# Performance work log

Hardware: AMD Instinct MI355X
Metric: run time of the kernel (lower is better)

The kernel has to match this reference:

```python
import jax, jax.numpy as jnp
import numpy as np
from jax.scipy.special import logsumexp

N, T, C, H, V = 8, 512, 1024, 256, 32000


def _res_layer(x, W1, b1, W2, b2):
    # hmm-lm ResLayer: x + ReLU(Linear(ReLU(Linear(x))))
    return x + jax.nn.relu(jax.nn.relu(x @ W1.T + b1) @ W2.T + b2)


def setup_inputs() -> dict:
    key = jax.random.key(0)
    ks = jax.random.split(key, 12)
    g = lambda k, shape: jax.random.normal(k, shape, jnp.float32) * (1.0 / np.sqrt(shape[-1]))
    return {
        "text": jax.random.randint(ks[0], (N, T), 0, V),
        "start_emb": jax.random.normal(ks[1], (H,), jnp.float32),
        "start_lin_W": g(ks[2], (H, H)),
        "start_lin_b": jnp.zeros((H,), jnp.float32),
        "start_res_W1": g(ks[3], (2, H, H)),
        "start_res_b1": jnp.zeros((2, H), jnp.float32),
        "start_res_W2": g(ks[4], (2, H, H)),
        "start_res_b2": jnp.zeros((2, H), jnp.float32),
        "state_emb": g(ks[5], (C, H)),
        "next_state_emb": g(ks[6], (C, H)),
        "preterminal_emb": g(ks[7], (C, H)),
        "term_res_W1": g(ks[8], (2, H, H)),
        "term_res_b1": jnp.zeros((2, H), jnp.float32),
        "term_res_W2": g(ks[9], (2, H, H)),
        "term_res_b2": jnp.zeros((2, H), jnp.float32),
        "terminal_emb": g(ks[10], (V, H)),
    }


def reference(text, start_emb, start_lin_W, start_lin_b,
              start_res_W1, start_res_b1, start_res_W2, start_res_b2,
              state_emb, next_state_emb, preterminal_emb,
              term_res_W1, term_res_b1, term_res_W2, term_res_b2,
              terminal_emb):
    # --- start distribution: start_mlp(start_emb) @ next_state_emb.T (tie_start) ---
    fx = start_emb @ start_lin_W.T + start_lin_b
    for i in range(2):
        fx = _res_layer(fx, start_res_W1[i], start_res_b1[i], start_res_W2[i], start_res_b2[i])
    start = jax.nn.log_softmax(fx @ next_state_emb.T)            # [C]

    # --- transition: log_softmax(state_emb @ next_state_emb.T) ---
    transition = jax.nn.log_softmax(state_emb @ next_state_emb.T, axis=-1)  # [C, C]

    # --- emission: log_softmax(terminal_mlp(preterminal_emb) @ terminal_emb.T) ---
    ft = preterminal_emb
    for i in range(2):
        ft = _res_layer(ft, term_res_W1[i], term_res_b1[i], term_res_W2[i], term_res_b2[i])
    emission = jax.nn.log_softmax(ft @ terminal_emb.T, axis=-1)  # [C, V]
    emis_t = emission.T                                          # [V, C]

    # --- HMM forward (log-space) scan; evidence = logsumexp(alpha_T) summed over batch ---
    alpha0 = start[None, :] + emis_t[text[:, 0]]                 # [N, C]

    def step(alpha, x_t):
        # alpha: [N, C]; x_t: [N]
        a = logsumexp(alpha[:, :, None] + transition[None], axis=1) + emis_t[x_t]
        return a, None

    alpha_T, _ = jax.lax.scan(step, alpha0, text[:, 1:].T)       # time-major [T-1, N]
    evidence = logsumexp(alpha_T, axis=-1).sum()
    return evidence
```

## Files before the change

kernel.cpp:

```cpp
#include <hip/hip_runtime.h>
#include <stdint.h>
#include <stddef.h>

#define N_ 8
#define T_ 512
#define C_ 1024
#define H_ 256
#define V_ 32000

#define OFF_START   0u
#define OFF_LSE     4096u
#define OFF_EVP     8192u
#define OFF_FT      81920u
#define OFF_P       1130496u
#define OFF_PART    5324800u
#define OFF_EEXP    5849088u
#define OFF_BUF     22626304u
#define OFF_FLAGS   22724608u

typedef __attribute__((ext_vector_type(8))) short short8;
typedef __attribute__((ext_vector_type(4))) float floatx4;

__device__ __forceinline__ float dot4(float4 a, float4 b) {
  return a.x*b.x + a.y*b.y + a.z*b.z + a.w*b.w;
}

__device__ __forceinline__ unsigned short f2bf(float f) {
  unsigned u = __float_as_uint(f);
  unsigned r = u + 0x7fffu + ((u >> 16) & 1u);
  return (unsigned short)(r >> 16);
}

__device__ __forceinline__ unsigned pk_bf2(float x, float y) {
  return ((unsigned)f2bf(y) << 16) | (unsigned)f2bf(x);
}

__device__ __forceinline__ short8 pack8(float4 a, float4 b) {
  union { short8 s; unsigned u[4]; } r;
  r.u[0] = pk_bf2(a.x, a.y);
  r.u[1] = pk_bf2(a.z, a.w);
  r.u[2] = pk_bf2(b.x, b.y);
  r.u[3] = pk_bf2(b.z, b.w);
  return r.s;
}

__global__ __launch_bounds__(256) void k_start(
    const float* __restrict__ se, const float* __restrict__ lw, const float* __restrict__ lb,
    const float* __restrict__ W1, const float* __restrict__ b1,
    const float* __restrict__ W2, const float* __restrict__ b2,
    const float* __restrict__ nse, float* __restrict__ out_start)
{
  __shared__ float xs[H_], fx[H_], h1[H_];
  __shared__ float lg[C_];
  __shared__ float redk[4];
  int tid = threadIdx.x;
  xs[tid] = se[tid];
  __syncthreads();
  {
    float acc = lb[tid];
    const float4* wr = (const float4*)(lw + (size_t)tid*H_);
    for (int k = 0; k < H_/4; ++k) acc += dot4(wr[k], *(const float4*)&xs[k*4]);
    fx[tid] = acc;
  }
  __syncthreads();
  for (int L = 0; L < 2; ++L) {
    {
      float acc = b1[L*H_ + tid];
      const float4* wr = (const float4*)(W1 + (size_t)(L*H_ + tid)*H_);
      for (int k = 0; k < H_/4; ++k) acc += dot4(wr[k], *(const float4*)&fx[k*4]);
      h1[tid] = fmaxf(acc, 0.f);
    }
    __syncthreads();
    {
      float acc = b2[L*H_ + tid];
      const float4* wr = (const float4*)(W2 + (size_t)(L*H_ + tid)*H_);
      for (int k = 0; k < H_/4; ++k) acc += dot4(wr[k], *(const float4*)&h1[k*4]);
      fx[tid] += fmaxf(acc, 0.f);
    }
    __syncthreads();
  }
  float lmax = -1e30f;
  for (int r = 0; r < 4; ++r) {
    int cc = tid + r*256;
    float acc = 0.f;
    const float4* er = (const float4*)(nse + (size_t)cc*H_);
    for (int k = 0; k < H_/4; ++k) acc += dot4(er[k], *(const float4*)&fx[k*4]);
    lg[cc] = acc;
    lmax = fmaxf(lmax, acc);
  }
  for (int m = 32; m; m >>= 1) lmax = fmaxf(lmax, __shfl_xor(lmax, m, 64));
  if ((tid & 63) == 0) redk[tid >> 6] = lmax;
  __syncthreads();
  float M = fmaxf(fmaxf(redk[0], redk[1]), fmaxf(redk[2], redk[3]));
  __syncthreads();
  float ssum = 0.f;
  for (int r = 0; r < 4; ++r) ssum += __expf(lg[tid + r*256] - M);
  for (int m = 32; m; m >>= 1) ssum += __shfl_xor(ssum, m, 64);
  if ((tid & 63) == 0) redk[tid >> 6] = ssum;
  __syncthreads();
  float S = redk[0] + redk[1] + redk[2] + redk[3];
  float lse = M + __logf(S);
  for (int r = 0; r < 4; ++r) {
    int cc = tid + r*256;
    out_start[cc] = lg[cc] - lse;
  }
}

__global__ __launch_bounds__(256) void k_gemm_cc(
    const float* __restrict__ A, const float* __restrict__ B, float* __restrict__ Cout)
{
  __shared__ float As[64][69];
  __shared__ float Bs[64][69];
  int tid = threadIdx.x;
  int bi = blockIdx.y, bj = blockIdx.x;
  int sr = tid >> 2, sq = tid & 3;
  int tx = tid & 15, ty = tid >> 4;
  float acc[4][4] = {};
  for (int kb = 0; kb < H_; kb += 64) {
    __syncthreads();
    {
      const float* ar = A + (size_t)(bi*64 + sr)*H_ + kb + sq*16;
      const float* br = B + (size_t)(bj*64 + sr)*H_ + kb + sq*16;
#pragma unroll
      for (int qq = 0; qq < 4; ++qq) {
        float4 av = *(const float4*)(ar + qq*4);
        float4 bv = *(const float4*)(br + qq*4);
        int kk = sq*16 + qq*4;
        As[sr][kk+0]=av.x; As[sr][kk+1]=av.y; As[sr][kk+2]=av.z; As[sr][kk+3]=av.w;
        Bs[sr][kk+0]=bv.x; Bs[sr][kk+1]=bv.y; Bs[sr][kk+2]=bv.z; Bs[sr][kk+3]=bv.w;
      }
    }
    __syncthreads();
#pragma unroll 4
    for (int k = 0; k < 64; ++k) {
      float a0 = As[ty*4+0][k], a1 = As[ty*4+1][k], a2 = As[ty*4+2][k], a3 = As[ty*4+3][k];
      float b0 = Bs[tx*4+0][k], b1 = Bs[tx*4+1][k], b2 = Bs[tx*4+2][k], b3 = Bs[tx*4+3][k];
      acc[0][0]+=a0*b0; acc[0][1]+=a0*b1; acc[0][2]+=a0*b2; acc[0][3]+=a0*b3;
      acc[1][0]+=a1*b0; acc[1][1]+=a1*b1; acc[1][2]+=a1*b2; acc[1][3]+=a1*b3;
      acc[2][0]+=a2*b0; acc[2][1]+=a2*b1; acc[2][2]+=a2*b2; acc[2][3]+=a2*b3;
      acc[3][0]+=a3*b0; acc[3][1]+=a3*b1; acc[3][2]+=a3*b2; acc[3][3]+=a3*b3;
    }
  }
#pragma unroll
  for (int ii = 0; ii < 4; ++ii)
#pragma unroll
    for (int jj = 0; jj < 4; ++jj)
      Cout[(size_t)(bi*64 + ty*4 + ii)*C_ + bj*64 + tx*4 + jj] = acc[ii][jj];
}

__global__ __launch_bounds__(256) void k_softmax_rows(float* __restrict__ P)
{
  __shared__ float redk[4];
  int row = blockIdx.x, tid = threadIdx.x;
  float4* pr = (float4*)(P + (size_t)row*C_);
  float4 v = pr[tid];
  float m = fmaxf(fmaxf(v.x, v.y), fmaxf(v.z, v.w));
  for (int mm = 32; mm; mm >>= 1) m = fmaxf(m, __shfl_xor(m, mm, 64));
  if ((tid & 63) == 0) redk[tid >> 6] = m;
  __syncthreads();
  float M = fmaxf(fmaxf(redk[0], redk[1]), fmaxf(redk[2], redk[3]));
  __syncthreads();
  float4 e;
  e.x = __expf(v.x - M); e.y = __expf(v.y - M); e.z = __expf(v.z - M); e.w = __expf(v.w - M);
  float s = e.x + e.y + e.z + e.w;
  for (int mm = 32; mm; mm >>= 1) s += __shfl_xor(s, mm, 64);
  if ((tid & 63) == 0) redk[tid >> 6] = s;
  __syncthreads();
  float S = redk[0] + redk[1] + redk[2] + redk[3];
  float inv = 1.0f / S;
  e.x *= inv; e.y *= inv; e.z *= inv; e.w *= inv;
  pr[tid] = e;
}

__global__ __launch_bounds__(256) void k_mlp(
    const float* __restrict__ inp, const float* __restrict__ W1, const float* __restrict__ b1,
    const float* __restrict__ W2, const float* __restrict__ b2, float* __restrict__ ft)
{
  __shared__ float xs[4][H_];
  __shared__ float hs[4][H_];
  int tid = threadIdx.x;
  int r0 = blockIdx.x * 4;
  int lr = tid >> 6, lc = (tid & 63) * 4;
  *(float4*)&xs[lr][lc] = *(const float4*)(inp + (size_t)(r0+lr)*H_ + lc);
  __syncthreads();
  for (int L = 0; L < 2; ++L) {
    {
      const float4* wr = (const float4*)(W1 + (size_t)(L*H_ + tid)*H_);
      float bb = b1[L*H_ + tid];
      float a0=bb, a1=bb, a2=bb, a3=bb;
      for (int k = 0; k < H_/4; ++k) {
        float4 w = wr[k];
        a0 += dot4(w, *(const float4*)&xs[0][k*4]);
        a1 += dot4(w, *(const float4*)&xs[1][k*4]);
        a2 += dot4(w, *(const float4*)&xs[2][k*4]);
        a3 += dot4(w, *(const float4*)&xs[3][k*4]);
      }
      hs[0][tid]=fmaxf(a0,0.f); hs[1][tid]=fmaxf(a1,0.f);
      hs[2][tid]=fmaxf(a2,0.f); hs[3][tid]=fmaxf(a3,0.f);
    }
    __syncthreads();
    {
      const float4* wr = (const float4*)(W2 + (size_t)(L*H_ + tid)*H_);
      float bb = b2[L*H_ + tid];
      float a0=bb, a1=bb, a2=bb, a3=bb;
      for (int k = 0; k < H_/4; ++k) {
        float4 w = wr[k];
        a0 += dot4(w, *(const float4*)&hs[0][k*4]);
        a1 += dot4(w, *(const float4*)&hs[1][k*4]);
        a2 += dot4(w, *(const float4*)&hs[2][k*4]);
        a3 += dot4(w, *(const float4*)&hs[3][k*4]);
      }
      xs[0][tid] += fmaxf(a0,0.f); xs[1][tid] += fmaxf(a1,0.f);
      xs[2][tid] += fmaxf(a2,0.f); xs[3][tid] += fmaxf(a3,0.f);
    }
    __syncthreads();
  }
  *(float4*)(ft + (size_t)(r0+lr)*H_ + lc) = *(float4*)&xs[lr][lc];
}

#define LSE_VSPLIT 16
#define LSE_VPB    2000
#define LSE_CHUNKS 125

__global__ __launch_bounds__(256) void k_lse_mfma(
    const float* __restrict__ ft, const float* __restrict__ emb, float* __restrict__ part)
{
  int tid = threadIdx.x;
  int lane = tid & 63;
  int w = tid >> 6;
  int q = blockIdx.x;
  int jb = blockIdx.y * 64 + w * 16;
  int r16 = lane & 15, kb = lane >> 4;

  short8 A[8];
  {
    const float* arow = ft + (size_t)(jb + r16) * H_ + kb * 8;
#pragma unroll
    for (int ks = 0; ks < 8; ++ks) {
      float4 a = *(const float4*)(arow + ks * 32);
      float4 b = *(const float4*)(arow + ks * 32 + 4);
      A[ks] = pack8(a, b);
    }
  }
  float s0 = 0.f, s1 = 0.f, s2 = 0.f, s3 = 0.f;
  const float* embq = emb + (size_t)q * LSE_VPB * H_;
#pragma unroll 1
  for (int ch = 0; ch < LSE_CHUNKS; ++ch) {
    const float* brow = embq + (size_t)(ch * 16 + r16) * H_ + kb * 8;
    floatx4 acca = {0,0,0,0}, accb = {0,0,0,0};
#pragma unroll
    for (int ks = 0; ks < 8; ks += 2) {
      float4 x0 = *(const float4*)(brow + ks * 32);
      float4 y0 = *(const float4*)(brow + ks * 32 + 4);
      float4 x1 = *(const float4*)(brow + ks * 32 + 32);
      float4 y1 = *(const float4*)(brow + ks * 32 + 36);
      acca = __builtin_amdgcn_mfma_f32_16x16x32_bf16(A[ks],   pack8(x0, y0), acca, 0, 0, 0);
      accb = __builtin_amdgcn_mfma_f32_16x16x32_bf16(A[ks+1], pack8(x1, y1), accb, 0, 0, 0);
    }
    s0 += __expf(acca[0] + accb[0]);
    s1 += __expf(acca[1] + accb[1]);
    s2 += __expf(acca[2] + accb[2]);
    s3 += __expf(acca[3] + accb[3]);
  }
#pragma unroll
  for (int mm = 1; mm <= 8; mm <<= 1) {
    s0 += __shfl_xor(s0, mm, 64);
    s1 += __shfl_xor(s1, mm, 64);
    s2 += __shfl_xor(s2, mm, 64);
    s3 += __shfl_xor(s3, mm, 64);
  }
  if (r16 == 0) {
    int jrow = jb + kb * 4;
    part[(size_t)(jrow + 0) * LSE_VSPLIT + q] = s0;
    part[(size_t)(jrow + 1) * LSE_VSPLIT + q] = s1;
    part[(size_t)(jrow + 2) * LSE_VSPLIT + q] = s2;
    part[(size_t)(jrow + 3) * LSE_VSPLIT + q] = s3;
  }
}

__global__ __launch_bounds__(256) void k_lse_reduce(
    const float* __restrict__ part, float* __restrict__ lse_row)
{
  int row = blockIdx.x * 256 + threadIdx.x;
  const float4* p = (const float4*)(part + (size_t)row * LSE_VSPLIT);
  float4 a = p[0], b = p[1], c = p[2], d = p[3];
  float s = a.x+a.y+a.z+a.w + b.x+b.y+b.z+b.w + c.x+c.y+c.z+c.w + d.x+d.y+d.z+d.w;
  lse_row[row] = __logf(s);
}

__global__ __launch_bounds__(256) void k_eexp_mfma(
    const float* __restrict__ ft, const float* __restrict__ emb, const int* __restrict__ text,
    const float* __restrict__ lse_row, float* __restrict__ EEXP)
{
  int tid = threadIdx.x;
  int lane = tid & 63;
  int w = tid >> 6;
  int jb = blockIdx.y * 64 + w * 16;
  int tb = blockIdx.x * 64;
  int r16 = lane & 15, kb = lane >> 4;

  short8 A[8];
  {
    const float* arow = ft + (size_t)(jb + r16) * H_ + kb * 8;
#pragma unroll
    for (int ks = 0; ks < 8; ++ks) {
      float4 a = *(const float4*)(arow + ks * 32);
      float4 b = *(const float4*)(arow + ks * 32 + 4);
      A[ks] = pack8(a, b);
    }
  }
  float4 lsej = *(const float4*)(lse_row + jb + kb * 4);

#pragma unroll 1
  for (int tc = 0; tc < 4; ++tc) {
    int idx = tb + tc * 16 + r16;
    int tok = text[idx];
    const float* brow = emb + (size_t)tok * H_ + kb * 8;
    floatx4 acca = {0,0,0,0}, accb = {0,0,0,0};
#pragma unroll
    for (int ks = 0; ks < 8; ks += 2) {
      float4 x0 = *(const float4*)(brow + ks * 32);
      float4 y0 = *(const float4*)(brow + ks * 32 + 4);
      float4 x1 = *(const float4*)(brow + ks * 32 + 32);
      float4 y1 = *(const float4*)(brow + ks * 32 + 36);
      acca = __builtin_amdgcn_mfma_f32_16x16x32_bf16(A[ks],   pack8(x0, y0), acca, 0, 0, 0);
      accb = __builtin_amdgcn_mfma_f32_16x16x32_bf16(A[ks+1], pack8(x1, y1), accb, 0, 0, 0);
    }
    float4 o;
    o.x = __expf(acca[0] + accb[0] - lsej.x);
    o.y = __expf(acca[1] + accb[1] - lsej.y);
    o.z = __expf(acca[2] + accb[2] - lsej.z);
    o.w = __expf(acca[3] + accb[3] - lsej.w);
    *(float4*)(EEXP + (size_t)idx * C_ + jb + kb * 4) = o;
  }
}

#define SCAN_LDS 136352

__global__ __launch_bounds__(256) void k_scan(
    const float* __restrict__ P, const float* __restrict__ EEXP, const float* __restrict__ startv,
    float* __restrict__ bufG, unsigned* __restrict__ flagsG, float* __restrict__ evp)
{
  extern __shared__ char smem[];
  char*  Pl   = smem;
  char*  Pr   = smem + 65536;
  char*  Al   = smem + 131072;
  float* red  = (float*)(smem + 135168);
  char*  Ub   = smem + 136192;
  float* redm = (float*)(smem + 136320);

  int tid  = threadIdx.x;
  int bid  = blockIdx.x;
  int c    = bid >> 2;
  int ng   = bid & 3;
  int n0   = ng * 2;
  int lane = tid & 63;
  int w    = tid >> 6;
  int s    = tid >> 7;
  int k0   = (tid & 127) * 8;
  int r16  = lane & 15, kb = lane >> 4;
  int j0   = r16;
  int jswz = j0 << 4;

  unsigned* myflags = flagsG + ng*32;
  float* bufq[3];
  bufq[0] = bufG + (size_t)(0*4 + ng)*2048;
  bufq[1] = bufG + (size_t)(1*4 + ng)*2048;
  bufq[2] = bufG + (size_t)(2*4 + ng)*2048;

  {
    int j4 = (tid & 7) * 4;
    int irow = tid >> 3;
    for (int rep = 0; rep < 32; ++rep) {
      int i = rep*32 + irow;
      float4 v = *(const float4*)(P + (size_t)i*C_ + c*32 + j4);
      int ib = 2*i;
      *(unsigned short*)(Pl + (size_t)(j4+0)*2048 + (ib ^ (((j4+0)&15)<<4))) = f2bf(v.x);
      *(unsigned short*)(Pl + (size_t)(j4+1)*2048 + (ib ^ (((j4+1)&15)<<4))) = f2bf(v.y);
      *(unsigned short*)(Pl + (size_t)(j4+2)*2048 + (ib ^ (((j4+2)&15)<<4))) = f2bf(v.z);
      *(unsigned short*)(Pl + (size_t)(j4+3)*2048 + (ib ^ (((j4+3)&15)<<4))) = f2bf(v.w);
    }
  }
  {
    int jb4 = (tid & 255) * 4;
    for (int m = 0; m < 32; ++m) {
      float4 v = *(const float4*)(P + (size_t)(c*32 + m)*C_ + jb4);
#pragma unroll
      for (int dj = 0; dj < 4; ++dj) {
        int j = jb4 + dj;
        float vv = (dj==0)?v.x:(dj==1)?v.y:(dj==2)?v.z:v.w;
        *(unsigned short*)(Pr + (size_t)(j>>4)*1024 + (j&15)*64 + m*2) = f2bf(vv);
      }
    }
  }

  float ls = 0.f;

#pragma unroll 1
  for (int r = 0; r < 256; ++r) {
    float ue = 0.f;
    if (tid < 64) {
      int ss = tid >> 5, col = tid & 31;
      ue = EEXP[((size_t)(n0+ss)*T_ + (2*r+1))*C_ + c*32 + col];
    }

    float av[8];
    if (r == 0) {
#pragma unroll
      for (int j = 0; j < 8; ++j)
        av[j] = __expf(startv[k0+j]) * EEXP[((size_t)(n0+s)*T_ + 0)*C_ + k0+j];
    } else {
      int guard = 0;
      for (;;) {
        unsigned f = (lane < 32)
          ? __hip_atomic_load(myflags + lane, __ATOMIC_RELAXED, __HIP_MEMORY_SCOPE_AGENT)
          : (unsigned)r;
        if (__ballot(f == (unsigned)r) == ~0ull) break;
        __builtin_amdgcn_s_sleep(1);
        if (++guard > 2000000) break;
      }
      float* srcb = bufq[(r-1)%3] + s*1024 + k0;
      float sv[8];
#pragma unroll
      for (int j = 0; j < 8; ++j)
        sv[j] = __hip_atomic_load(srcb + j, __ATOMIC_RELAXED, __HIP_MEMORY_SCOPE_AGENT);
      float4 e0 = *(const float4*)(EEXP + ((size_t)(n0+s)*T_ + 2*r)*C_ + k0);
      float4 e1 = *(const float4*)(EEXP + ((size_t)(n0+s)*T_ + 2*r)*C_ + k0 + 4);
      av[0]=sv[0]*e0.x; av[1]=sv[1]*e0.y; av[2]=sv[2]*e0.z; av[3]=sv[3]*e0.w;
      av[4]=sv[4]*e1.x; av[5]=sv[5]*e1.y; av[6]=sv[6]*e1.z; av[7]=sv[7]*e1.w;
      if (tid < 64) {
        int ss = tid >> 5, col = tid & 31;
        __hip_atomic_store(bufq[(r+1)%3] + ss*1024 + c*32 + col, 0.0f,
                           __ATOMIC_RELAXED, __HIP_MEMORY_SCOPE_AGENT);
      }
    }

    float m = fmaxf(fmaxf(fmaxf(av[0],av[1]),fmaxf(av[2],av[3])),
                    fmaxf(fmaxf(av[4],av[5]),fmaxf(av[6],av[7])));
#pragma unroll
    for (int mm = 1; mm <= 32; mm <<= 1) m = fmaxf(m, __shfl_xor(m, mm, 64));
    if (lane == 0) redm[w] = m;
    __syncthreads();
    float M = fmaxf(redm[s*2], redm[s*2+1]);
    ls += __logf(M);
    float rinv = 1.0f / M;
    {
      unsigned pk[4];
      pk[0] = pk_bf2(av[0]*rinv, av[1]*rinv);
      pk[1] = pk_bf2(av[2]*rinv, av[3]*rinv);
      pk[2] = pk_bf2(av[4]*rinv, av[5]*rinv);
      pk[3] = pk_bf2(av[6]*rinv, av[7]*rinv);
      int blk = k0 >> 5;
      *(uint4*)(Al + blk*128 + s*64 + (((k0&31)*2) ^ ((blk&3)<<4))) = *(const uint4*)pk;
    }
    __syncthreads();

    floatx4 acc0 = {0,0,0,0}, acc1 = {0,0,0,0};
#pragma unroll
    for (int b = 0; b < 8; ++b) {
      int blk = w*8 + b;
      short8 af = *(const short8*)(Al + blk*128 + (r16&1)*64 + ((kb*16) ^ ((blk&3)<<4)));
      int kby = 2*(blk*32 + kb*8);
      short8 f0 = *(const short8*)(Pl + (size_t)j0*2048 + (kby ^ jswz));
      short8 f1 = *(const short8*)(Pl + (size_t)(16+j0)*2048 + (kby ^ jswz));
      acc0 = __builtin_amdgcn_mfma_f32_16x16x32_bf16(af, f0, acc0, 0, 0, 0);
      acc1 = __builtin_amdgcn_mfma_f32_16x16x32_bf16(af, f1, acc1, 0, 0, 0);
    }
    if (lane < 16) {
      red[((w*2+0)*2+0)*16 + j0] = acc0[0];
      red[((w*2+0)*2+1)*16 + j0] = acc0[1];
      red[((w*2+1)*2+0)*16 + j0] = acc1[0];
      red[((w*2+1)*2+1)*16 + j0] = acc1[1];
    }
    __syncthreads();

    if (r == 255) {
      if (tid < 64) {
        int ss = tid >> 5, col = tid & 31;
        int tl = col >> 4, c16 = col & 15;
        float usum = red[((0*2+tl)*2+ss)*16 + c16] + red[((1*2+tl)*2+ss)*16 + c16]
                   + red[((2*2+tl)*2+ss)*16 + c16] + red[((3*2+tl)*2+ss)*16 + c16];
        (void)__hip_atomic_fetch_add(bufq[255%3] + ss*1024 + c*32 + col, usum * ue,
                                     __ATOMIC_RELAXED, __HIP_MEMORY_SCOPE_AGENT);
      }
      __syncthreads();
      if (tid == 0)
        __hip_atomic_store(myflags + c, 256u, __ATOMIC_RELAXED, __HIP_MEMORY_SCOPE_AGENT);
    } else {
      if (tid < 64) {
        int ss = tid >> 5, col = tid & 31;
        int tl = col >> 4, c16 = col & 15;
        float usum = red[((0*2+tl)*2+ss)*16 + c16] + red[((1*2+tl)*2+ss)*16 + c16]
                   + red[((2*2+tl)*2+ss)*16 + c16] + red[((3*2+tl)*2+ss)*16 + c16];
        *(unsigned short*)(Ub + ss*64 + col*2) = f2bf(usum * ue);
      }
      __syncthreads();
      short8 au = *(const short8*)(Ub + (r16&1)*64 + kb*16);
      float* bufp = bufq[r%3];
#pragma unroll 4
      for (int i = 0; i < 16; ++i) {
        int jt = w*16 + i;
        short8 bf = *(const short8*)(Pr + (size_t)jt*1024 + j0*64 + kb*16);
        floatx4 a = {0,0,0,0};
        a = __builtin_amdgcn_mfma_f32_16x16x32_bf16(au, bf, a, 0, 0, 0);
        if (lane < 16) {
          (void)__hip_atomic_fetch_add(bufp + 0*1024 + jt*16 + j0, a[0],
                                       __ATOMIC_RELAXED, __HIP_MEMORY_SCOPE_AGENT);
          (void)__hip_atomic_fetch_add(bufp + 1*1024 + jt*16 + j0, a[1],
                                       __ATOMIC_RELAXED, __HIP_MEMORY_SCOPE_AGENT);
        }
      }
      __syncthreads();
      if (tid == 0)
        __hip_atomic_store(myflags + c, (unsigned)(r+1), __ATOMIC_RELAXED, __HIP_MEMORY_SCOPE_AGENT);
    }
  }

  if (c == 0) {
    int guard = 0;
    for (;;) {
      unsigned f = (lane < 32)
        ? __hip_atomic_load(myflags + lane, __ATOMIC_RELAXED, __HIP_MEMORY_SCOPE_AGENT)
        : 256u;
      if (__ballot(f == 256u) == ~0ull) break;
      __builtin_amdgcn_s_sleep(1);
      if (++guard > 2000000) break;
    }
    float* srcb = bufq[255%3] + s*1024 + k0;
    float ssum = 0.f;
#pragma unroll
    for (int j = 0; j < 8; ++j)
      ssum += __hip_atomic_load(srcb + j, __ATOMIC_RELAXED, __HIP_MEMORY_SCOPE_AGENT);
#pragma unroll
    for (int mm = 1; mm <= 32; mm <<= 1) ssum += __shfl_xor(ssum, mm, 64);
    if (lane == 0) redm[w] = ssum;
    __syncthreads();
    if (tid == 0)   evp[n0]     = ls + __logf(redm[0] + redm[1]);
    if (tid == 128) evp[n0 + 1] = ls + __logf(redm[2] + redm[3]);
  }
}

__global__ void k_final(const float* __restrict__ evp, float* __restrict__ out)
{
  if (threadIdx.x == 0) {
    float s = 0.f;
#pragma unroll
    for (int i = 0; i < N_; ++i) s += evp[i];
    out[0] = s;
  }
}

extern "C" void kernel_launch(void* const* d_in, const int* in_sizes, int n_in,
                              void* d_out, int out_size, void* d_ws, size_t ws_size,
                              hipStream_t stream)
{
  const int*   text      = (const int*)  d_in[0];
  const float* start_emb = (const float*)d_in[1];
  const float* slw       = (const float*)d_in[2];
  const float* slb       = (const float*)d_in[3];
  const float* sW1       = (const float*)d_in[4];
  const float* sb1       = (const float*)d_in[5];
  const float* sW2       = (const float*)d_in[6];
  const float* sb2       = (const float*)d_in[7];
  const float* state_emb = (const float*)d_in[8];
  const float* nse       = (const float*)d_in[9];
  const float* pre_emb   = (const float*)d_in[10];
  const float* tW1       = (const float*)d_in[11];
  const float* tb1       = (const float*)d_in[12];
  const float* tW2       = (const float*)d_in[13];
  const float* tb2       = (const float*)d_in[14];
  const float* term_emb  = (const float*)d_in[15];

  char* ws = (char*)d_ws;
  float*    w_start = (float*)   (ws + OFF_START);
  float*    w_lse   = (float*)   (ws + OFF_LSE);
  float*    w_evp   = (float*)   (ws + OFF_EVP);
  float*    w_ft    = (float*)   (ws + OFF_FT);
  float*    w_P     = (float*)   (ws + OFF_P);
  float*    w_part  = (float*)   (ws + OFF_PART);
  float*    w_eexp  = (float*)   (ws + OFF_EEXP);
  float*    w_buf   = (float*)   (ws + OFF_BUF);
  unsigned* w_flags = (unsigned*)(ws + OFF_FLAGS);

  (void)hipMemsetAsync(ws + OFF_BUF, 0, 98304 + 512, stream);

  k_start<<<1, 256, 0, stream>>>(start_emb, slw, slb, sW1, sb1, sW2, sb2, nse, w_start);
  k_gemm_cc<<<dim3(16,16), 256, 0, stream>>>(state_emb, nse, w_P);
  k_softmax_rows<<<C_, 256, 0, stream>>>(w_P);
  k_mlp<<<C_/4, 256, 0, stream>>>(pre_emb, tW1, tb1, tW2, tb2, w_ft);
  k_lse_mfma<<<dim3(LSE_VSPLIT, 16), 256, 0, stream>>>(w_ft, term_emb, w_part);
  k_lse_reduce<<<4, 256, 0, stream>>>(w_part, w_lse);
  k_eexp_mfma<<<dim3(64, 16), 256, 0, stream>>>(w_ft, term_emb, text, w_lse, w_eexp);

  (void)hipFuncSetAttribute((const void*)k_scan, hipFuncAttributeMaxDynamicSharedMemorySize, SCAN_LDS);
  k_scan<<<128, 256, SCAN_LDS, stream>>>(w_P, w_eexp, w_start, w_buf, w_flags, w_evp);
  k_final<<<1, 64, 0, stream>>>(w_evp, (float*)d_out);
}
```

Before: 1.654 ms.

## Halve scan blocks, pre-pack transposed bf16 transition, use counter barrier and deferred max

Adds a kernel that writes the softmaxed transition matrix as a transposed bf16 copy. The scan now runs on 64 blocks of 64 columns each instead of 128 blocks of 32, and loads its slices straight from that copy. The right-hand operand is held in registers rather than LDS. The per-block flag array becomes a single atomic counter per batch group, and normalisation uses the previous step's max so one block-wide sync leaves the critical path. Fewer blocks cut the cross-block synchronisation cost per step, but each block does twice the work, and register pressure goes up from the 32 short8 register fragments.

```diff
diff --git a/kernel.cpp b/kernel.cpp
--- a/kernel.cpp
+++ b/kernel.cpp
@@ -16,7 +16,8 @@
 #define OFF_PART    5324800u
 #define OFF_EEXP    5849088u
 #define OFF_BUF     22626304u
-#define OFF_FLAGS   22724608u
+#define OFF_CNT     22724608u
+#define OFF_PT      22725120u
 
 typedef __attribute__((ext_vector_type(8))) short short8;
 typedef __attribute__((ext_vector_type(4))) float floatx4;
@@ -170,6 +171,32 @@
   float inv = 1.0f / S;
   e.x *= inv; e.y *= inv; e.z *= inv; e.w *= inv;
   pr[tid] = e;
+}
+
+__global__ __launch_bounds__(256) void k_packT(
+    const float* __restrict__ P, unsigned short* __restrict__ PT)
+{
+  __shared__ float ts[64][68];
+  int tid = threadIdx.x;
+  int bi = blockIdx.y, bj = blockIdx.x;
+  int rl = tid >> 4;
+  int cl4 = (tid & 15) * 4;
+#pragma unroll
+  for (int rr = 0; rr < 4; ++rr) {
+    int row = rr*16 + rl;
+    float4 v = *(const float4*)(P + (size_t)(bi*64 + row)*C_ + bj*64 + cl4);
+    ts[row][cl4+0]=v.x; ts[row][cl4+1]=v.y; ts[row][cl4+2]=v.z; ts[row][cl4+3]=v.w;
+  }
+  __syncthreads();
+  int jl = tid >> 2;
+  int m0 = (tid & 3) * 16;
+  unsigned pk[8];
+#pragma unroll
+  for (int u = 0; u < 8; ++u)
+    pk[u] = pk_bf2(ts[m0 + u*2][jl], ts[m0 + u*2 + 1][jl]);
+  char* dst = (char*)(PT + (size_t)(bj*64 + jl)*1024 + bi*64 + m0);
+  *(uint4*)(dst +  0) = *(const uint4*)&pk[0];
+  *(uint4*)(dst + 16) = *(const uint4*)&pk[4];
 }
 
 __global__ __launch_bounds__(256) void k_mlp(
@@ -335,19 +362,18 @@
   }
 }
 
-#define SCAN_LDS 136352
+#define SCAN_LDS (131072 + 4096 + 256 + 32)
 
 __global__ __launch_bounds__(256) void k_scan(
-    const float* __restrict__ P, const float* __restrict__ EEXP, const float* __restrict__ startv,
-    float* __restrict__ bufG, unsigned* __restrict__ flagsG, float* __restrict__ evp)
+    const unsigned short* __restrict__ PT, const float* __restrict__ EEXP,
+    const float* __restrict__ startv,
+    float* __restrict__ bufG, unsigned* __restrict__ cntG, float* __restrict__ evp)
 {
   extern __shared__ char smem[];
   char*  Pl   = smem;
-  char*  Pr   = smem + 65536;
   char*  Al   = smem + 131072;
-  float* red  = (float*)(smem + 135168);
-  char*  Ub   = smem + 136192;
-  float* redm = (float*)(smem + 136320);
+  char*  Ub   = smem + 135168;
+  float* redm = (float*)(smem + 135424);
 
   int tid  = threadIdx.x;
   int bid  = blockIdx.x;
@@ -358,92 +384,90 @@
   int w    = tid >> 6;
   int s    = tid >> 7;
   int k0   = (tid & 127) * 8;
-  int r16  = lane & 15, kb = lane >> 4;
-  int j0   = r16;
-  int jswz = j0 << 4;
-
-  unsigned* myflags = flagsG + ng*32;
+  int r16  = lane & 15;
+  int kb4  = lane >> 4;
+
+  unsigned* cnt = cntG + ng * 16;
   float* bufq[3];
   bufq[0] = bufG + (size_t)(0*4 + ng)*2048;
   bufq[1] = bufG + (size_t)(1*4 + ng)*2048;
   bufq[2] = bufG + (size_t)(2*4 + ng)*2048;
 
   {
-    int j4 = (tid & 7) * 4;
-    int irow = tid >> 3;
-    for (int rep = 0; rep < 32; ++rep) {
-      int i = rep*32 + irow;
-      float4 v = *(const float4*)(P + (size_t)i*C_ + c*32 + j4);
-      int ib = 2*i;
-      *(unsigned short*)(Pl + (size_t)(j4+0)*2048 + (ib ^ (((j4+0)&15)<<4))) = f2bf(v.x);
-      *(unsigned short*)(Pl + (size_t)(j4+1)*2048 + (ib ^ (((j4+1)&15)<<4))) = f2bf(v.y);
-      *(unsigned short*)(Pl + (size_t)(j4+2)*2048 + (ib ^ (((j4+2)&15)<<4))) = f2bf(v.z);
-      *(unsigned short*)(Pl + (size_t)(j4+3)*2048 + (ib ^ (((j4+3)&15)<<4))) = f2bf(v.w);
-    }
-  }
-  {
-    int jb4 = (tid & 255) * 4;
-    for (int m = 0; m < 32; ++m) {
-      float4 v = *(const float4*)(P + (size_t)(c*32 + m)*C_ + jb4);
-#pragma unroll
-      for (int dj = 0; dj < 4; ++dj) {
-        int j = jb4 + dj;
-        float vv = (dj==0)?v.x:(dj==1)?v.y:(dj==2)?v.z:v.w;
-        *(unsigned short*)(Pr + (size_t)(j>>4)*1024 + (j&15)*64 + m*2) = f2bf(vv);
-      }
-    }
-  }
-
-  float ls = 0.f;
+    int col = tid & 63, q = tid >> 6;
+    const char* src = (const char*)(PT + (size_t)(c*64 + col)*1024) + q*512;
+    char* dstb = Pl + (size_t)col*2048;
+    int swz = (col & 15) << 4;
+#pragma unroll
+    for (int u = 0; u < 32; ++u)
+      *(uint4*)(dstb + ((q*512 + u*16) ^ swz)) = *(const uint4*)(src + u*16);
+  }
+
+  short8 vb[16][2];
+#pragma unroll
+  for (int i = 0; i < 16; ++i)
+#pragma unroll
+    for (int q = 0; q < 2; ++q)
+      vb[i][q] = *(const short8*)((const char*)PT +
+          ((size_t)((w*16 + i)*16 + r16)*1024 + c*64 + q*32 + kb4*8)*2);
+
+  __syncthreads();
+
+  float ls   = 0.f;
+  float Muse = 1.f;
+  int s2   = r16 & 1;
+  int ucol = c*64 + w*16 + r16;
 
 #pragma unroll 1
   for (int r = 0; r < 256; ++r) {
-    float ue = 0.f;
-    if (tid < 64) {
-      int ss = tid >> 5, col = tid & 31;
-      ue = EEXP[((size_t)(n0+ss)*T_ + (2*r+1))*C_ + c*32 + col];
-    }
+    float ue0 = 0.f, ue1 = 0.f;
+    if (lane < 16) {
+      ue0 = EEXP[((size_t)(n0+0)*T_ + (2*r+1))*C_ + ucol];
+      ue1 = EEXP[((size_t)(n0+1)*T_ + (2*r+1))*C_ + ucol];
+    }
+    float4 e0 = *(const float4*)(EEXP + ((size_t)(n0+s)*T_ + 2*r)*C_ + k0);
+    float4 e1 = *(const float4*)(EEXP + ((size_t)(n0+s)*T_ + 2*r)*C_ + k0 + 4);
 
     float av[8];
     if (r == 0) {
-#pragma unroll
-      for (int j = 0; j < 8; ++j)
-        av[j] = __expf(startv[k0+j]) * EEXP[((size_t)(n0+s)*T_ + 0)*C_ + k0+j];
+      av[0] = __expf(startv[k0+0]) * e0.x;
+      av[1] = __expf(startv[k0+1]) * e0.y;
+      av[2] = __expf(startv[k0+2]) * e0.z;
+      av[3] = __expf(startv[k0+3]) * e0.w;
+      av[4] = __expf(startv[k0+4]) * e1.x;
+      av[5] = __expf(startv[k0+5]) * e1.y;
+      av[6] = __expf(startv[k0+6]) * e1.z;
+      av[7] = __expf(startv[k0+7]) * e1.w;
     } else {
+      unsigned tgt = 16u * (unsigned)r;
       int guard = 0;
       for (;;) {
-        unsigned f = (lane < 32)
-          ? __hip_atomic_load(myflags + lane, __ATOMIC_RELAXED, __HIP_MEMORY_SCOPE_AGENT)
-          : (unsigned)r;
-        if (__ballot(f == (unsigned)r) == ~0ull) break;
+        unsigned f = __hip_atomic_load(cnt, __ATOMIC_RELAXED, __HIP_MEMORY_SCOPE_AGENT);
+        if (f >= tgt) break;
         __builtin_amdgcn_s_sleep(1);
-        if (++guard > 2000000) break;
+        if (++guard > 4000000) break;
       }
       float* srcb = bufq[(r-1)%3] + s*1024 + k0;
       float sv[8];
 #pragma unroll
       for (int j = 0; j < 8; ++j)
         sv[j] = __hip_atomic_load(srcb + j, __ATOMIC_RELAXED, __HIP_MEMORY_SCOPE_AGENT);
-      float4 e0 = *(const float4*)(EEXP + ((size_t)(n0+s)*T_ + 2*r)*C_ + k0);
-      float4 e1 = *(const float4*)(EEXP + ((size_t)(n0+s)*T_ + 2*r)*C_ + k0 + 4);
       av[0]=sv[0]*e0.x; av[1]=sv[1]*e0.y; av[2]=sv[2]*e0.z; av[3]=sv[3]*e0.w;
       av[4]=sv[4]*e1.x; av[5]=sv[5]*e1.y; av[6]=sv[6]*e1.z; av[7]=sv[7]*e1.w;
-      if (tid < 64) {
-        int ss = tid >> 5, col = tid & 31;
-        __hip_atomic_store(bufq[(r+1)%3] + ss*1024 + c*32 + col, 0.0f,
+      if (tid < 128) {
+        int ss = tid >> 6, col = c*64 + (tid & 63);
+        __hip_atomic_store(bufq[(r+1)%3] + ss*1024 + col, 0.0f,
                            __ATOMIC_RELAXED, __HIP_MEMORY_SCOPE_AGENT);
       }
     }
 
-    float m = fmaxf(fmaxf(fmaxf(av[0],av[1]),fmaxf(av[2],av[3])),
-                    fmaxf(fmaxf(av[4],av[5]),fmaxf(av[6],av[7])));
-#pragma unroll
-    for (int mm = 1; mm <= 32; mm <<= 1) m = fmaxf(m, __shfl_xor(m, mm, 64));
-    if (lane == 0) redm[w] = m;
-    __syncthreads();
-    float M = fmaxf(redm[s*2], redm[s*2+1]);
-    ls += __logf(M);
-    float rinv = 1.0f / M;
+    ls += __logf(Muse);
+    float rinv = 1.0f / Muse;
+    float m8 = fmaxf(fmaxf(fmaxf(av[0],av[1]),fmaxf(av[2],av[3])),
+                     fmaxf(fmaxf(av[4],av[5]),fmaxf(av[6],av[7])));
+#pragma unroll
+    for (int mm = 1; mm <= 32; mm <<= 1) m8 = fmaxf(m8, __shfl_xor(m8, mm, 64));
+    if (lane == 0) redm[w] = m8;
     {
       unsigned pk[4];
       pk[0] = pk_bf2(av[0]*rinv, av[1]*rinv);
@@ -454,79 +478,73 @@
       *(uint4*)(Al + blk*128 + s*64 + (((k0&31)*2) ^ ((blk&3)<<4))) = *(const uint4*)pk;
     }
     __syncthreads();
-
-    floatx4 acc0 = {0,0,0,0}, acc1 = {0,0,0,0};
-#pragma unroll
-    for (int b = 0; b < 8; ++b) {
-      int blk = w*8 + b;
-      short8 af = *(const short8*)(Al + blk*128 + (r16&1)*64 + ((kb*16) ^ ((blk&3)<<4)));
-      int kby = 2*(blk*32 + kb*8);
-      short8 f0 = *(const short8*)(Pl + (size_t)j0*2048 + (kby ^ jswz));
-      short8 f1 = *(const short8*)(Pl + (size_t)(16+j0)*2048 + (kby ^ jswz));
-      acc0 = __builtin_amdgcn_mfma_f32_16x16x32_bf16(af, f0, acc0, 0, 0, 0);
-      acc1 = __builtin_amdgcn_mfma_f32_16x16x32_bf16(af, f1, acc1, 0, 0, 0);
-    }
-    if (lane < 16) {
-      red[((w*2+0)*2+0)*16 + j0] = acc0[0];
-      red[((w*2+0)*2+1)*16 + j0] = acc0[1];
-      red[((w*2+1)*2+0)*16 + j0] = acc1[0];
-      red[((w*2+1)*2+1)*16 + j0] = acc1[1];
-    }
-    __syncthreads();
+    Muse = fmaxf(fmaxf(redm[0], redm[1]), fmaxf(redm[2], redm[3])) * rinv;
+
+    floatx4 acc[4] = {{0,0,0,0},{0,0,0,0},{0,0,0,0},{0,0,0,0}};
+    {
+      const char* bcol = Pl + (size_t)(w*16 + r16)*2048;
+      int swzc = r16 << 4;
+#pragma unroll
+      for (int ch = 0; ch < 4; ++ch)
+#pragma unroll
+        for (int b8 = 0; b8 < 8; ++b8) {
+          int blk = b8*4 + ch;
+          short8 af = *(const short8*)(Al + blk*128 + s2*64 + ((kb4*16) ^ ((blk&3)<<4)));
+          short8 bf = *(const short8*)(bcol + ((blk*64 + kb4*16) ^ swzc));
+          acc[ch] = __builtin_amdgcn_mfma_f32_16x16x32_bf16(af, bf, acc[ch], 0, 0, 0);
+        }
+    }
+    floatx4 us;
+    us[0] = (acc[0][0]+acc[1][0]) + (acc[2][0]+acc[3][0]);
+    us[1] = (acc[0][1]+acc[1][1]) + (acc[2][1]+acc[3][1]);
 
     if (r == 255) {
-      if (tid < 64) {
-        int ss = tid >> 5, col = tid & 31;
-        int tl = col >> 4, c16 = col & 15;
-        float usum = red[((0*2+tl)*2+ss)*16 + c16] + red[((1*2+tl)*2+ss)*16 + c16]
-                   + red[((2*2+tl)*2+ss)*16 + c16] + red[((3*2+tl)*2+ss)*16 + c16];
-        (void)__hip_atomic_fetch_add(bufq[255%3] + ss*1024 + c*32 + col, usum * ue,
+      if (lane < 16) {
+        (void)__hip_atomic_fetch_add(bufq[0] + 0*1024 + ucol, us[0]*ue0,
+                                     __ATOMIC_RELAXED, __HIP_MEMORY_SCOPE_AGENT);
+        (void)__hip_atomic_fetch_add(bufq[0] + 1*1024 + ucol, us[1]*ue1,
                                      __ATOMIC_RELAXED, __HIP_MEMORY_SCOPE_AGENT);
       }
       __syncthreads();
       if (tid == 0)
-        __hip_atomic_store(myflags + c, 256u, __ATOMIC_RELAXED, __HIP_MEMORY_SCOPE_AGENT);
+        (void)__hip_atomic_fetch_add(cnt, 1u, __ATOMIC_RELAXED, __HIP_MEMORY_SCOPE_AGENT);
     } else {
-      if (tid < 64) {
-        int ss = tid >> 5, col = tid & 31;
-        int tl = col >> 4, c16 = col & 15;
-        float usum = red[((0*2+tl)*2+ss)*16 + c16] + red[((1*2+tl)*2+ss)*16 + c16]
-                   + red[((2*2+tl)*2+ss)*16 + c16] + red[((3*2+tl)*2+ss)*16 + c16];
-        *(unsigned short*)(Ub + ss*64 + col*2) = f2bf(usum * ue);
+      if (lane < 16) {
+        *(unsigned short*)(Ub + 0*128 + (w*16 + r16)*2) = f2bf(us[0] * ue0);
+        *(unsigned short*)(Ub + 1*128 + (w*16 + r16)*2) = f2bf(us[1] * ue1);
       }
       __syncthreads();
-      short8 au = *(const short8*)(Ub + (r16&1)*64 + kb*16);
+      short8 ua0 = *(const short8*)(Ub + s2*128 +  0 + kb4*16);
+      short8 ua1 = *(const short8*)(Ub + s2*128 + 64 + kb4*16);
       float* bufp = bufq[r%3];
-#pragma unroll 4
+#pragma unroll
       for (int i = 0; i < 16; ++i) {
-        int jt = w*16 + i;
-        short8 bf = *(const short8*)(Pr + (size_t)jt*1024 + j0*64 + kb*16);
         floatx4 a = {0,0,0,0};
-        a = __builtin_amdgcn_mfma_f32_16x16x32_bf16(au, bf, a, 0, 0, 0);
+        a = __builtin_amdgcn_mfma_f32_16x16x32_bf16(ua0, vb[i][0], a, 0, 0, 0);
+        a = __builtin_amdgcn_mfma_f32_16x16x32_bf16(ua1, vb[i][1], a, 0, 0, 0);
         if (lane < 16) {
-          (void)__hip_atomic_fetch_add(bufp + 0*1024 + jt*16 + j0, a[0],
+          int jc = (w*16 + i)*16 + r16;
+          (void)__hip_atomic_fetch_add(bufp + jc, a[0],
                                        __ATOMIC_RELAXED, __HIP_MEMORY_SCOPE_AGENT);
-          (void)__hip_atomic_fetch_add(bufp + 1*1024 + jt*16 + j0, a[1],
+          (void)__hip_atomic_fetch_add(bufp + 1024 + jc, a[1],
                                        __ATOMIC_RELAXED, __HIP_MEMORY_SCOPE_AGENT);
         }
       }
       __syncthreads();
       if (tid == 0)
-        __hip_atomic_store(myflags + c, (unsigned)(r+1), __ATOMIC_RELAXED, __HIP_MEMORY_SCOPE_AGENT);
+        (void)__hip_atomic_fetch_add(cnt, 1u, __ATOMIC_RELAXED, __HIP_MEMORY_SCOPE_AGENT);
     }
   }
 
   if (c == 0) {
     int guard = 0;
     for (;;) {
-      unsigned f = (lane < 32)
-        ? __hip_atomic_load(myflags + lane, __ATOMIC_RELAXED, __HIP_MEMORY_SCOPE_AGENT)
-        : 256u;
-      if (__ballot(f == 256u) == ~0ull) break;
+      unsigned f = __hip_atomic_load(cnt, __ATOMIC_RELAXED, __HIP_MEMORY_SCOPE_AGENT);
+      if (f >= 4096u) break;
       __builtin_amdgcn_s_sleep(1);
-      if (++guard > 2000000) break;
-    }
-    float* srcb = bufq[255%3] + s*1024 + k0;
+      if (++guard > 4000000) break;
+    }
+    float* srcb = bufq[0] + s*1024 + k0;
     float ssum = 0.f;
 #pragma unroll
     for (int j = 0; j < 8; ++j)
@@ -572,27 +590,29 @@
   const float* term_emb  = (const float*)d_in[15];
 
   char* ws = (char*)d_ws;
-  float*    w_start = (float*)   (ws + OFF_START);
-  float*    w_lse   = (float*)   (ws + OFF_LSE);
-  float*    w_evp   = (float*)   (ws + OFF_EVP);
-  float*    w_ft    = (float*)   (ws + OFF_FT);
-  float*    w_P     = (float*)   (ws + OFF_P);
-  float*    w_part  = (float*)   (ws + OFF_PART);
-  float*    w_eexp  = (float*)   (ws + OFF_EEXP);
-  float*    w_buf   = (float*)   (ws + OFF_BUF);
-  unsigned* w_flags = (unsigned*)(ws + OFF_FLAGS);
+  float*          w_start = (float*)         (ws + OFF_START);
+  float*          w_lse   = (float*)         (ws + OFF_LSE);
+  float*          w_evp   = (float*)         (ws + OFF_EVP);
+  float*          w_ft    = (float*)         (ws + OFF_FT);
+  float*          w_P     = (float*)         (ws + OFF_P);
+  float*          w_part  = (float*)         (ws + OFF_PART);
+  float*          w_eexp  = (float*)         (ws + OFF_EEXP);
+  float*          w_buf   = (float*)         (ws + OFF_BUF);
+  unsigned*       w_cnt   = (unsigned*)      (ws + OFF_CNT);
+  unsigned short* w_pt    = (unsigned short*)(ws + OFF_PT);
 
   (void)hipMemsetAsync(ws + OFF_BUF, 0, 98304 + 512, stream);
 
   k_start<<<1, 256, 0, stream>>>(start_emb, slw, slb, sW1, sb1, sW2, sb2, nse, w_start);
   k_gemm_cc<<<dim3(16,16), 256, 0, stream>>>(state_emb, nse, w_P);
   k_softmax_rows<<<C_, 256, 0, stream>>>(w_P);
+  k_packT<<<dim3(16,16), 256, 0, stream>>>(w_P, w_pt);
   k_mlp<<<C_/4, 256, 0, stream>>>(pre_emb, tW1, tb1, tW2, tb2, w_ft);
   k_lse_mfma<<<dim3(LSE_VSPLIT, 16), 256, 0, stream>>>(w_ft, term_emb, w_part);
   k_lse_reduce<<<4, 256, 0, stream>>>(w_part, w_lse);
   k_eexp_mfma<<<dim3(64, 16), 256, 0, stream>>>(w_ft, term_emb, text, w_lse, w_eexp);
 
   (void)hipFuncSetAttribute((const void*)k_scan, hipFuncAttributeMaxDynamicSharedMemorySize, SCAN_LDS);
-  k_scan<<<128, 256, SCAN_LDS, stream>>>(w_P, w_eexp, w_start, w_buf, w_flags, w_evp);
+  k_scan<<<64, 256, SCAN_LDS, stream>>>(w_pt, w_eexp, w_start, w_buf, w_cnt, w_evp);
   k_final<<<1, 64, 0, stream>>>(w_evp, (float*)d_out);
 }
```

Result: faster. 1.612 ms, median of 2 (-2.5%).
